# Optimization experiments

Measured on AMD Instinct MI355X. Metric: run time of the kernel, lower is better.

The kernel has to match this reference:

```python
import jax, jax.numpy as jnp
import numpy as np
from jax import lax

B, A, C, M = 8, 100000, 80, 32
ALPHA, GAMMA = 0.25, 2.0


def _calc_iou(a, b):
    # a: [A,4] anchors, b: [M,4] gt boxes -> [A,M]
    area = (b[:, 2] - b[:, 0]) * (b[:, 3] - b[:, 1])
    iw = jnp.clip(jnp.minimum(a[:, None, 2], b[None, :, 2]) - jnp.maximum(a[:, None, 0], b[None, :, 0]), 0.0)
    ih = jnp.clip(jnp.minimum(a[:, None, 3], b[None, :, 3]) - jnp.maximum(a[:, None, 1], b[None, :, 1]), 0.0)
    inter = iw * ih
    ua = jnp.clip(((a[:, 2] - a[:, 0]) * (a[:, 3] - a[:, 1]))[:, None] + area[None, :] - inter, 1e-8)
    return inter / ua


def _per_image(cls_p, reg, ann, anchor):
    # cls_p: [A,C], reg: [A,4], ann: [M,9], anchor: [A,4]
    p = jnp.clip(cls_p, 1e-4, 1.0 - 1e-4)
    iou = _calc_iou(anchor, ann[:, :4])            # [A,M]
    iou_max = jnp.max(iou, axis=1)                 # [A]
    iou_arg = jnp.argmax(iou, axis=1)              # [A]
    assigned = ann[iou_arg]                        # [A,9]
    pos = iou_max >= 0.5
    num_pos = jnp.sum(pos)

    # targets: -1 = ignore, 0 = background, one-hot for positives
    t = jnp.where(iou_max[:, None] < 0.4, 0.0, -1.0)
    cls_idx = lax.stop_gradient(assigned[:, 4]).astype(jnp.int32)
    t = jnp.where(pos[:, None], jax.nn.one_hot(cls_idx, C, dtype=p.dtype), t)

    alpha_f = jnp.where(t == 1.0, ALPHA, 1.0 - ALPHA)
    fw = jnp.where(t == 1.0, 1.0 - p, p)
    bce = -(t * jnp.log(p) + (1.0 - t) * jnp.log(1.0 - p))
    cls_loss = jnp.where(t != -1.0, alpha_f * fw ** GAMMA * bce, 0.0)
    cls_l = jnp.sum(cls_loss) / jnp.maximum(num_pos.astype(p.dtype), 1.0)

    aw = anchor[:, 2] - anchor[:, 0]
    ah = anchor[:, 3] - anchor[:, 1]
    acx = anchor[:, 0] + 0.5 * aw
    acy = anchor[:, 1] + 0.5 * ah
    gw_raw = assigned[:, 2] - assigned[:, 0]
    gh_raw = assigned[:, 3] - assigned[:, 1]
    gcx = assigned[:, 0] + 0.5 * gw_raw
    gcy = assigned[:, 1] + 0.5 * gh_raw
    gw = jnp.clip(gw_raw, 1.0)
    gh = jnp.clip(gh_raw, 1.0)
    tgt = jnp.stack([(gcx - acx) / aw, (gcy - acy) / ah,
                     jnp.log(gw / aw), jnp.log(gh / ah)], axis=1)
    tgt = tgt / jnp.array([0.1, 0.1, 0.2, 0.2], dtype=p.dtype)
    diff = jnp.abs(tgt - reg)
    sl1 = jnp.where(diff <= 1.0 / 9.0, 0.5 * 9.0 * diff ** 2, diff - 0.5 / 9.0)
    denom = jnp.maximum(num_pos.astype(p.dtype) * 4.0, 1.0)
    reg_l = jnp.where(num_pos > 0,
                      jnp.sum(jnp.where(pos[:, None], sl1, 0.0)) / denom,
                      jnp.zeros((), p.dtype))
    return cls_l, reg_l


def setup_inputs() -> dict:
    key = jax.random.key(0)
    k = jax.random.split(key, 8)
    classifications = jax.random.uniform(k[0], (B, A, C), jnp.float32, 1e-3, 1.0 - 1e-3)
    regressions = 0.1 * jax.random.normal(k[1], (B, A, 4), jnp.float32)
    ax0 = jax.random.uniform(k[2], (A,), jnp.float32, 0.0, 900.0)
    ay0 = jax.random.uniform(k[3], (A,), jnp.float32, 0.0, 900.0)
    awh = jax.random.uniform(k[4], (A, 2), jnp.float32, 16.0, 128.0)
    anchors = jnp.stack([ax0, ay0, ax0 + awh[:, 0], ay0 + awh[:, 1]], axis=1)[None]
    b0 = jax.random.uniform(k[5], (B, M, 2), jnp.float32, 0.0, 800.0)
    bwh = jax.random.uniform(k[6], (B, M, 2), jnp.float32, 8.0, 200.0)
    labels = jax.random.randint(k[7], (B, M, 1), 0, C).astype(jnp.float32)
    extra = jnp.zeros((B, M, 4), jnp.float32)  # cols 5..8: instance id + geo filler
    annotations = jnp.concatenate([b0, b0 + bwh, labels, extra], axis=-1)  # [B,M,9]
    return dict(classifications=classifications, regressions=regressions,
                anchors=anchors, annotations=annotations)


def reference(classifications, regressions, anchors, annotations):
    anchor = anchors[0]
    cls_l, reg_l = jax.vmap(_per_image, in_axes=(0, 0, 0, None))(
        classifications, regressions, annotations, anchor)
    return jnp.stack([jnp.mean(cls_l), jnp.mean(reg_l)])
```

## Files before the change

kernel.cpp:

```cpp
#include <hip/hip_runtime.h>

#define A_N 100000
#define B_N 8
#define C_N 80
#define M_N 32

typedef float vfloat4 __attribute__((ext_vector_type(4)));


__global__ __launch_bounds__(256) void focal_main(
    const vfloat4* __restrict__ cls4,
    const float4* __restrict__ reg4,
    const float4* __restrict__ anc4,
    const float*  __restrict__ ann,
    float* __restrict__ cls_sum, float* __restrict__ reg_sum, int* __restrict__ npos)
{
    __shared__ float annL[M_N][6];
    __shared__ int   metaL[256];
    __shared__ float redA[4];
    __shared__ int   redI[4];
    __shared__ float redB[4];

    const int b   = blockIdx.y;
    const int a0  = blockIdx.x * 256;
    const int tid = threadIdx.x;

    for (int i = tid; i < M_N * 5; i += 256) {
        int m = i / 5, c = i % 5;
        annL[m][c] = ann[(b * M_N + m) * 9 + c];
    }
    __syncthreads();
    if (tid < M_N) {
        annL[tid][5] = (annL[tid][2] - annL[tid][0]) * (annL[tid][3] - annL[tid][1]);
    }
    __syncthreads();

    const int a = a0 + tid;
    const bool valid = a < A_N;
    float regacc = 0.0f;
    bool pos = false;
    int st = 1;
    int ci = 0;

    if (valid) {
        float4 an = anc4[a];
        float aw = an.z - an.x, ah = an.w - an.y;
        float aArea = aw * ah;
        float best = -1.0f; int bidx = 0;
        #pragma unroll 8
        for (int m = 0; m < M_N; ++m) {
            float iw = fminf(an.z, annL[m][2]) - fmaxf(an.x, annL[m][0]);
            float ih = fminf(an.w, annL[m][3]) - fmaxf(an.y, annL[m][1]);
            iw = fmaxf(iw, 0.0f); ih = fmaxf(ih, 0.0f);
            float inter = iw * ih;
            float ua = fmaxf(aArea + annL[m][5] - inter, 1e-8f);
            float iou = inter / ua;
            if (iou > best) { best = iou; bidx = m; }
        }
        pos = best >= 0.5f;
        st  = pos ? 2 : (best < 0.4f ? 0 : 1);
        ci  = (int)annL[bidx][4];

        if (pos) {
            float4 r = reg4[(size_t)b * A_N + a];
            float gx0 = annL[bidx][0], gy0 = annL[bidx][1];
            float gx1 = annL[bidx][2], gy1 = annL[bidx][3];
            float gwr = gx1 - gx0, ghr = gy1 - gy0;
            float gcx = gx0 + 0.5f * gwr, gcy = gy0 + 0.5f * ghr;
            float gw = fmaxf(gwr, 1.0f), gh = fmaxf(ghr, 1.0f);
            float acx = an.x + 0.5f * aw, acy = an.y + 0.5f * ah;
            float t0 = (gcx - acx) / aw * 10.0f;
            float t1 = (gcy - acy) / ah * 10.0f;
            float t2 = __logf(gw / aw) * 5.0f;
            float t3 = __logf(gh / ah) * 5.0f;
            float d0 = fabsf(t0 - r.x), d1 = fabsf(t1 - r.y);
            float d2 = fabsf(t2 - r.z), d3 = fabsf(t3 - r.w);
            const float th = 1.0f / 9.0f;
            const float hs = 0.5f / 9.0f;
            regacc  = (d0 <= th) ? 4.5f * d0 * d0 : d0 - hs;
            regacc += (d1 <= th) ? 4.5f * d1 * d1 : d1 - hs;
            regacc += (d2 <= th) ? 4.5f * d2 * d2 : d2 - hs;
            regacc += (d3 <= th) ? 4.5f * d3 * d3 : d3 - hs;
        }
    }
    metaL[tid] = st | (ci << 2);

    unsigned long long bal = __ballot(pos);
    #pragma unroll
    for (int o = 32; o > 0; o >>= 1) regacc += __shfl_down(regacc, o, 64);
    int lane = tid & 63, wid = tid >> 6;
    if (lane == 0) { redA[wid] = regacc; redI[wid] = __popcll(bal); }
    __syncthreads();
    if (tid == 0) {
        float rs = redA[0] + redA[1] + redA[2] + redA[3];
        int   np = redI[0] + redI[1] + redI[2] + redI[3];
        if (rs != 0.0f) atomicAdd(&reg_sum[b], rs);
        if (np)         atomicAdd(&npos[b], np);
    }

    const vfloat4* cbase = cls4 + ((size_t)b * A_N + a0) * 20;
    const int nA = min(256, A_N - a0);
    float clsacc = 0.0f;

    if (nA == 256) {
        #pragma unroll 4
        for (int k = 0; k < 20; ++k) {
            int i   = tid + (k << 8);
            vfloat4 v = __builtin_nontemporal_load(cbase + i);
            int la  = i / 20;
            int c0  = (i - la * 20) * 4;
            int m   = metaL[la];
            int st2 = m & 3;
            int ciL = m >> 2;
            float notIgn = (st2 != 1) ? 1.0f : 0.0f;
            bool  isPos  = (st2 == 2);
            float pv[4] = {v.x, v.y, v.z, v.w};
            float term = 0.0f;
            #pragma unroll
            for (int j = 0; j < 4; ++j) {
                float p = fminf(fmaxf(pv[j], 1e-4f), 1.0f - 1e-4f);
                bool one = isPos && (c0 + j == ciL);
                float alphaf = one ? 0.25f : 0.75f;
                float w      = one ? 1.0f - p : p;
                float arg    = one ? p : 1.0f - p;
                term += alphaf * w * w * (-__logf(arg));
            }
            clsacc += notIgn * term;
        }
    } else {
        const int n4 = nA * 20;
        for (int i = tid; i < n4; i += 256) {
            vfloat4 v = __builtin_nontemporal_load(cbase + i);
            int la  = i / 20;
            int c0  = (i - la * 20) * 4;
            int m   = metaL[la];
            int st2 = m & 3;
            int ciL = m >> 2;
            float notIgn = (st2 != 1) ? 1.0f : 0.0f;
            bool  isPos  = (st2 == 2);
            float pv[4] = {v.x, v.y, v.z, v.w};
            float term = 0.0f;
            #pragma unroll
            for (int j = 0; j < 4; ++j) {
                float p = fminf(fmaxf(pv[j], 1e-4f), 1.0f - 1e-4f);
                bool one = isPos && (c0 + j == ciL);
                float alphaf = one ? 0.25f : 0.75f;
                float w      = one ? 1.0f - p : p;
                float arg    = one ? p : 1.0f - p;
                term += alphaf * w * w * (-__logf(arg));
            }
            clsacc += notIgn * term;
        }
    }

    #pragma unroll
    for (int o = 32; o > 0; o >>= 1) clsacc += __shfl_down(clsacc, o, 64);
    if (lane == 0) redB[wid] = clsacc;
    __syncthreads();
    if (tid == 0) {
        float cs = redB[0] + redB[1] + redB[2] + redB[3];
        atomicAdd(&cls_sum[b], cs);
    }
}

__global__ void focal_finalize(const float* __restrict__ cls_sum,
                               const float* __restrict__ reg_sum,
                               const int* __restrict__ npos,
                               float* __restrict__ out)
{
    if (threadIdx.x == 0) {
        float c = 0.0f, r = 0.0f;
        for (int b = 0; b < B_N; ++b) {
            float np = (float)npos[b];
            c += cls_sum[b] / fmaxf(np, 1.0f);
            r += (npos[b] > 0) ? reg_sum[b] / (4.0f * np) : 0.0f;
        }
        out[0] = c / (float)B_N;
        out[1] = r / (float)B_N;
    }
}

extern "C" void kernel_launch(void* const* d_in, const int* in_sizes, int n_in,
                              void* d_out, int out_size, void* d_ws, size_t ws_size,
                              hipStream_t stream) {
    const float* cls = (const float*)d_in[0];
    const float* reg = (const float*)d_in[1];
    const float* anc = (const float*)d_in[2];
    const float* ann = (const float*)d_in[3];

    float* ws      = (float*)d_ws;
    float* cls_sum = ws;
    float* reg_sum = ws + 8;
    int*   npos    = (int*)(ws + 16);

    (void)hipMemsetAsync(d_ws, 0, 24 * sizeof(float), stream);

    dim3 grid((A_N + 255) / 256, B_N);
    focal_main<<<grid, 256, 0, stream>>>(
        (const vfloat4*)cls, (const float4*)reg, (const float4*)anc, ann,
        cls_sum, reg_sum, npos);

    focal_finalize<<<1, 64, 0, stream>>>(cls_sum, reg_sum, npos, (float*)d_out);
}
```

Measured before the change: 385.6 us.

## Simplify focal loss to background-log form and fuse finalize via ticket counter

The per-element focal loss now computes only the background term (0.75·p²·log(1−p)) for all four classes with one log each, and adds a positive-class correction only for the single matching class. The four select-heavy branches and the per-element choice of log argument go away. The separate finalize kernel is also removed: the last block to finish, found with an atomic ticket and thread fences, computes the final outputs. This saves one kernel launch at the cost of an extra atomic per block.

Result: slower. 504.8 us (+30.9%).

```diff
diff --git a/kernel.cpp b/kernel.cpp
--- a/kernel.cpp
+++ b/kernel.cpp
@@ -13,7 +13,9 @@
     const float4* __restrict__ reg4,
     const float4* __restrict__ anc4,
     const float*  __restrict__ ann,
-    float* __restrict__ cls_sum, float* __restrict__ reg_sum, int* __restrict__ npos)
+    float* __restrict__ cls_sum, float* __restrict__ reg_sum,
+    int* __restrict__ npos, int* __restrict__ ticket,
+    float* __restrict__ out)
 {
     __shared__ float annL[M_N][6];
     __shared__ int   metaL[256];
@@ -112,20 +114,25 @@
             int m   = metaL[la];
             int st2 = m & 3;
             int ciL = m >> 2;
-            float notIgn = (st2 != 1) ? 1.0f : 0.0f;
-            bool  isPos  = (st2 == 2);
-            float pv[4] = {v.x, v.y, v.z, v.w};
-            float term = 0.0f;
-            #pragma unroll
-            for (int j = 0; j < 4; ++j) {
-                float p = fminf(fmaxf(pv[j], 1e-4f), 1.0f - 1e-4f);
-                bool one = isPos && (c0 + j == ciL);
-                float alphaf = one ? 0.25f : 0.75f;
-                float w      = one ? 1.0f - p : p;
-                float arg    = one ? p : 1.0f - p;
-                term += alphaf * w * w * (-__logf(arg));
+            float scale = (st2 != 1) ? -0.75f : 0.0f;
+            float p0 = fminf(fmaxf(v.x, 1e-4f), 1.0f - 1e-4f);
+            float p1 = fminf(fmaxf(v.y, 1e-4f), 1.0f - 1e-4f);
+            float p2 = fminf(fmaxf(v.z, 1e-4f), 1.0f - 1e-4f);
+            float p3 = fminf(fmaxf(v.w, 1e-4f), 1.0f - 1e-4f);
+            float l0 = __logf(1.0f - p0);
+            float l1 = __logf(1.0f - p1);
+            float l2 = __logf(1.0f - p2);
+            float l3 = __logf(1.0f - p3);
+            float s4 = fmaf(p0 * p0, l0,
+                       fmaf(p1 * p1, l1,
+                       fmaf(p2 * p2, l2, p3 * p3 * l3)));
+            clsacc = fmaf(scale, s4, clsacc);
+            if (st2 == 2 && (unsigned)(ciL - c0) < 4u) {
+                int j = ciL - c0;
+                float pj = (j == 0) ? p0 : (j == 1) ? p1 : (j == 2) ? p2 : p3;
+                float qj = 1.0f - pj;
+                clsacc += -0.25f * qj * qj * __logf(pj) + 0.75f * pj * pj * __logf(qj);
             }
-            clsacc += notIgn * term;
         }
     } else {
         const int n4 = nA * 20;
@@ -136,20 +143,25 @@
             int m   = metaL[la];
             int st2 = m & 3;
             int ciL = m >> 2;
-            float notIgn = (st2 != 1) ? 1.0f : 0.0f;
-            bool  isPos  = (st2 == 2);
-            float pv[4] = {v.x, v.y, v.z, v.w};
-            float term = 0.0f;
-            #pragma unroll
-            for (int j = 0; j < 4; ++j) {
-                float p = fminf(fmaxf(pv[j], 1e-4f), 1.0f - 1e-4f);
-                bool one = isPos && (c0 + j == ciL);
-                float alphaf = one ? 0.25f : 0.75f;
-                float w      = one ? 1.0f - p : p;
-                float arg    = one ? p : 1.0f - p;
-                term += alphaf * w * w * (-__logf(arg));
+            float scale = (st2 != 1) ? -0.75f : 0.0f;
+            float p0 = fminf(fmaxf(v.x, 1e-4f), 1.0f - 1e-4f);
+            float p1 = fminf(fmaxf(v.y, 1e-4f), 1.0f - 1e-4f);
+            float p2 = fminf(fmaxf(v.z, 1e-4f), 1.0f - 1e-4f);
+            float p3 = fminf(fmaxf(v.w, 1e-4f), 1.0f - 1e-4f);
+            float l0 = __logf(1.0f - p0);
+            float l1 = __logf(1.0f - p1);
+            float l2 = __logf(1.0f - p2);
+            float l3 = __logf(1.0f - p3);
+            float s4 = fmaf(p0 * p0, l0,
+                       fmaf(p1 * p1, l1,
+                       fmaf(p2 * p2, l2, p3 * p3 * l3)));
+            clsacc = fmaf(scale, s4, clsacc);
+            if (st2 == 2 && (unsigned)(ciL - c0) < 4u) {
+                int j = ciL - c0;
+                float pj = (j == 0) ? p0 : (j == 1) ? p1 : (j == 2) ? p2 : p3;
+                float qj = 1.0f - pj;
+                clsacc += -0.25f * qj * qj * __logf(pj) + 0.75f * pj * pj * __logf(qj);
             }
-            clsacc += notIgn * term;
         }
     }
 
@@ -160,23 +172,23 @@
     if (tid == 0) {
         float cs = redB[0] + redB[1] + redB[2] + redB[3];
         atomicAdd(&cls_sum[b], cs);
-    }
-}
-
-__global__ void focal_finalize(const float* __restrict__ cls_sum,
-                               const float* __restrict__ reg_sum,
-                               const int* __restrict__ npos,
-                               float* __restrict__ out)
-{
-    if (threadIdx.x == 0) {
-        float c = 0.0f, r = 0.0f;
-        for (int b = 0; b < B_N; ++b) {
-            float np = (float)npos[b];
-            c += cls_sum[b] / fmaxf(np, 1.0f);
-            r += (npos[b] > 0) ? reg_sum[b] / (4.0f * np) : 0.0f;
-        }
-        out[0] = c / (float)B_N;
-        out[1] = r / (float)B_N;
+
+        __threadfence();
+        int t = atomicAdd(ticket, 1);
+        if (t == (int)(gridDim.x * gridDim.y) - 1) {
+            __threadfence();
+            float c = 0.0f, r = 0.0f;
+            #pragma unroll
+            for (int bb = 0; bb < B_N; ++bb) {
+                float np = (float)atomicAdd(&npos[bb], 0);
+                float cv = atomicAdd(&cls_sum[bb], 0.0f);
+                float rv = atomicAdd(&reg_sum[bb], 0.0f);
+                c += cv / fmaxf(np, 1.0f);
+                r += (np > 0.0f) ? rv / (4.0f * np) : 0.0f;
+            }
+            out[0] = c * (1.0f / B_N);
+            out[1] = r * (1.0f / B_N);
+        }
     }
 }
 
@@ -192,13 +204,12 @@
     float* cls_sum = ws;
     float* reg_sum = ws + 8;
     int*   npos    = (int*)(ws + 16);
-
-    (void)hipMemsetAsync(d_ws, 0, 24 * sizeof(float), stream);
+    int*   ticket  = (int*)(ws + 24);
+
+    (void)hipMemsetAsync(d_ws, 0, 32 * sizeof(float), stream);
 
     dim3 grid((A_N + 255) / 256, B_N);
     focal_main<<<grid, 256, 0, stream>>>(
         (const vfloat4*)cls, (const float4*)reg, (const float4*)anc, ann,
-        cls_sum, reg_sum, npos);
-
-    focal_finalize<<<1, 64, 0, stream>>>(cls_sum, reg_sum, npos, (float*)d_out);
+        cls_sum, reg_sum, npos, ticket, (float*)d_out);
 }
```

## Treat all classes as background and correct the positive class separately, batching loads

Applied to the files above, without the earlier changes.

The per-element focal term now always uses the background formula, scaled by a per-anchor factor held in shared memory. For each positive anchor, the thread then reads its one assigned-class probability, subtracting the background term and adding the foreground term. This removes per-element class comparisons and selects from the streaming loop. The fixed 20-iteration loop is also fully unrolled into two batches of ten nontemporal loads issued before the compute, which raises memory-level parallelism but costs more registers and adds one scattered load per positive anchor.

New measurement: 385.2 us. No clear change (-0.1%).

```diff
diff --git a/kernel.cpp b/kernel.cpp
--- a/kernel.cpp
+++ b/kernel.cpp
@@ -8,15 +8,28 @@
 typedef float vfloat4 __attribute__((ext_vector_type(4)));
 
 
+__device__ __forceinline__ float bg_s4(vfloat4 v) {
+    float p0 = fminf(fmaxf(v.x, 1e-4f), 1.0f - 1e-4f);
+    float p1 = fminf(fmaxf(v.y, 1e-4f), 1.0f - 1e-4f);
+    float p2 = fminf(fmaxf(v.z, 1e-4f), 1.0f - 1e-4f);
+    float p3 = fminf(fmaxf(v.w, 1e-4f), 1.0f - 1e-4f);
+    float l0 = __logf(1.0f - p0);
+    float l1 = __logf(1.0f - p1);
+    float l2 = __logf(1.0f - p2);
+    float l3 = __logf(1.0f - p3);
+    return fmaf(p0 * p0, l0, fmaf(p1 * p1, l1, fmaf(p2 * p2, l2, p3 * p3 * l3)));
+}
+
 __global__ __launch_bounds__(256) void focal_main(
     const vfloat4* __restrict__ cls4,
+    const float*  __restrict__ clsf,
     const float4* __restrict__ reg4,
     const float4* __restrict__ anc4,
     const float*  __restrict__ ann,
     float* __restrict__ cls_sum, float* __restrict__ reg_sum, int* __restrict__ npos)
 {
     __shared__ float annL[M_N][6];
-    __shared__ int   metaL[256];
+    __shared__ float scaleL[256];
     __shared__ float redA[4];
     __shared__ int   redI[4];
     __shared__ float redB[4];
@@ -38,9 +51,9 @@
     const int a = a0 + tid;
     const bool valid = a < A_N;
     float regacc = 0.0f;
+    float clsacc = 0.0f;
     bool pos = false;
     int st = 1;
-    int ci = 0;
 
     if (valid) {
         float4 an = anc4[a];
@@ -59,7 +72,6 @@
         }
         pos = best >= 0.5f;
         st  = pos ? 2 : (best < 0.4f ? 0 : 1);
-        ci  = (int)annL[bidx][4];
 
         if (pos) {
             float4 r = reg4[(size_t)b * A_N + a];
@@ -81,9 +93,15 @@
             regacc += (d1 <= th) ? 4.5f * d1 * d1 : d1 - hs;
             regacc += (d2 <= th) ? 4.5f * d2 * d2 : d2 - hs;
             regacc += (d3 <= th) ? 4.5f * d3 * d3 : d3 - hs;
+
+            int ci = (int)annL[bidx][4];
+            float pc = clsf[((size_t)b * A_N + a) * C_N + ci];
+            pc = fminf(fmaxf(pc, 1e-4f), 1.0f - 1e-4f);
+            float qc = 1.0f - pc;
+            clsacc = -0.25f * qc * qc * __logf(pc) + 0.75f * pc * pc * __logf(qc);
         }
     }
-    metaL[tid] = st | (ci << 2);
+    scaleL[tid] = (st != 1) ? -0.75f : 0.0f;
 
     unsigned long long bal = __ballot(pos);
     #pragma unroll
@@ -100,56 +118,30 @@
 
     const vfloat4* cbase = cls4 + ((size_t)b * A_N + a0) * 20;
     const int nA = min(256, A_N - a0);
-    float clsacc = 0.0f;
 
     if (nA == 256) {
-        #pragma unroll 4
-        for (int k = 0; k < 20; ++k) {
-            int i   = tid + (k << 8);
-            vfloat4 v = __builtin_nontemporal_load(cbase + i);
-            int la  = i / 20;
-            int c0  = (i - la * 20) * 4;
-            int m   = metaL[la];
-            int st2 = m & 3;
-            int ciL = m >> 2;
-            float notIgn = (st2 != 1) ? 1.0f : 0.0f;
-            bool  isPos  = (st2 == 2);
-            float pv[4] = {v.x, v.y, v.z, v.w};
-            float term = 0.0f;
-            #pragma unroll
-            for (int j = 0; j < 4; ++j) {
-                float p = fminf(fmaxf(pv[j], 1e-4f), 1.0f - 1e-4f);
-                bool one = isPos && (c0 + j == ciL);
-                float alphaf = one ? 0.25f : 0.75f;
-                float w      = one ? 1.0f - p : p;
-                float arg    = one ? p : 1.0f - p;
-                term += alphaf * w * w * (-__logf(arg));
-            }
-            clsacc += notIgn * term;
+        vfloat4 bufA[10], bufB[10];
+        #pragma unroll
+        for (int u = 0; u < 10; ++u)
+            bufA[u] = __builtin_nontemporal_load(cbase + tid + (u << 8));
+        #pragma unroll
+        for (int u = 0; u < 10; ++u)
+            bufB[u] = __builtin_nontemporal_load(cbase + tid + ((u + 10) << 8));
+        #pragma unroll
+        for (int u = 0; u < 10; ++u) {
+            int i = tid + (u << 8);
+            clsacc = fmaf(scaleL[i / 20], bg_s4(bufA[u]), clsacc);
+        }
+        #pragma unroll
+        for (int u = 0; u < 10; ++u) {
+            int i = tid + ((u + 10) << 8);
+            clsacc = fmaf(scaleL[i / 20], bg_s4(bufB[u]), clsacc);
         }
     } else {
         const int n4 = nA * 20;
         for (int i = tid; i < n4; i += 256) {
             vfloat4 v = __builtin_nontemporal_load(cbase + i);
-            int la  = i / 20;
-            int c0  = (i - la * 20) * 4;
-            int m   = metaL[la];
-            int st2 = m & 3;
-            int ciL = m >> 2;
-            float notIgn = (st2 != 1) ? 1.0f : 0.0f;
-            bool  isPos  = (st2 == 2);
-            float pv[4] = {v.x, v.y, v.z, v.w};
-            float term = 0.0f;
-            #pragma unroll
-            for (int j = 0; j < 4; ++j) {
-                float p = fminf(fmaxf(pv[j], 1e-4f), 1.0f - 1e-4f);
-                bool one = isPos && (c0 + j == ciL);
-                float alphaf = one ? 0.25f : 0.75f;
-                float w      = one ? 1.0f - p : p;
-                float arg    = one ? p : 1.0f - p;
-                term += alphaf * w * w * (-__logf(arg));
-            }
-            clsacc += notIgn * term;
+            clsacc = fmaf(scaleL[i / 20], bg_s4(v), clsacc);
         }
     }
 
@@ -197,7 +189,7 @@
 
     dim3 grid((A_N + 255) / 256, B_N);
     focal_main<<<grid, 256, 0, stream>>>(
-        (const vfloat4*)cls, (const float4*)reg, (const float4*)anc, ann,
+        (const vfloat4*)cls, cls, (const float4*)reg, (const float4*)anc, ann,
         cls_sum, reg_sum, npos);
 
     focal_finalize<<<1, 64, 0, stream>>>(cls_sum, reg_sum, npos, (float*)d_out);
```
